# Optimization experiments

Hardware: AMD Instinct MI355X
Metric: run time of the kernel (lower is better)

Reference implementation:

```python
import jax, jax.numpy as jnp
import numpy as np

IN_FEATURES = 4096
OUT_FEATURES = 4096
NUM_GROUPS = 32
HARDTANH_MIN = -2.0
HARDTANH_MAX = 2.0
EPS = 1e-6


def setup_inputs() -> dict:
    key = jax.random.key(0)
    k1, k2 = jax.random.split(key)
    x = jax.random.normal(k1, (8192, IN_FEATURES), dtype=jnp.float32)
    W = jax.random.normal(k2, (OUT_FEATURES, IN_FEATURES), dtype=jnp.float32)
    b = jnp.zeros((OUT_FEATURES,), dtype=jnp.float32)
    return {"x": x, "W": W, "b": b}


def reference(x, W, b):
    B = x.shape[0]
    group_size = OUT_FEATURES // NUM_GROUPS
    # GEMM: y[b, n] = sum_k x[b, k] * W[n, k]
    y = jnp.einsum("bk,nk->bn", x, W)
    # GroupNorm over each group of channels per row (no affine scale)
    yg = y.reshape(B, NUM_GROUPS, group_size)
    mean = jnp.mean(yg, axis=2, keepdims=True)
    var = jnp.mean((yg - mean) ** 2, axis=2, keepdims=True)
    norm = (yg - mean) / jnp.sqrt(var + EPS)
    norm = norm.reshape(B, OUT_FEATURES) + b[None, :]
    # kernel clamps to [-2, 2], then outer clamp to [hardtanh_min, hardtanh_max]
    out = jnp.clip(norm, -2.0, 2.0)
    out = jnp.clip(out, HARDTANH_MIN, HARDTANH_MAX)
    return out
```

## Files before the change

### kernel.cpp

```cpp
#include <hip/hip_runtime.h>
#include <hip/hip_bf16.h>
#include <stdint.h>

#define M_DIM 8192
#define N_DIM 4096
#define K_DIM 4096
#define BM 128
#define BN 128
#define BK 32

typedef __attribute__((ext_vector_type(8))) short short8;
typedef __attribute__((ext_vector_type(4))) float f32x4;
typedef unsigned short ushort_t;

__device__ __forceinline__ ushort_t f2bf(float f) {
    uint32_t u = __float_as_uint(f);
    uint32_t r = (u + 0x7FFFu + ((u >> 16) & 1u)) >> 16;
    return (ushort_t)r;
}

__global__ void cvt_f32_bf16(const float4* __restrict__ in, ushort* __restrict__ out4, int n4) {
    int i = blockIdx.x * blockDim.x + threadIdx.x;
    if (i < n4) {
        float4 v = in[i];
        ushort_t a = f2bf(v.x), b = f2bf(v.y), c = f2bf(v.z), d = f2bf(v.w);
        uint32_t lo = (uint32_t)a | ((uint32_t)b << 16);
        uint32_t hi = (uint32_t)c | ((uint32_t)d << 16);
        uint2* o = reinterpret_cast<uint2*>(out4);
        o[i] = make_uint2(lo, hi);
    }
}

__device__ __forceinline__ void gload_lds16(const ushort_t* g, ushort_t* l) {
    __builtin_amdgcn_global_load_lds(
        (const __attribute__((address_space(1))) unsigned int*)g,
        (__attribute__((address_space(3))) unsigned int*)l,
        16, 0, 0);
}

__global__ __launch_bounds__(256, 2)
void gemm_gn_kernel(const ushort_t* __restrict__ xb,
                    const ushort_t* __restrict__ wb,
                    const float*   __restrict__ bias,
                    float*         __restrict__ out)
{
    __shared__ ushort_t As[BM * BK];
    __shared__ ushort_t Bs[BN * BK];
    __shared__ float redS [2][BM];
    __shared__ float redS2[2][BM];

    const int tid = threadIdx.x;
    const int w   = tid >> 6;
    const int l   = tid & 63;
    const int wr  = w >> 1;
    const int wc  = w & 1;
    const int l15 = l & 15;
    const int l4  = l >> 4;

    const int TN   = N_DIM / BN;
    const int bid  = blockIdx.x;
    const int brow = (bid / TN) * BM;
    const int bcol = (bid % TN) * BN;

    f32x4 acc[4][4];
#pragma unroll
    for (int i = 0; i < 4; ++i)
#pragma unroll
        for (int j = 0; j < 4; ++j) acc[i][j] = (f32x4){0.f, 0.f, 0.f, 0.f};

    const int srow = tid >> 2;
    const int scol = (tid & 3) * 8;
    const ushort_t* ga0 = xb + (size_t)(brow + srow)      * K_DIM + scol;
    const ushort_t* ga1 = xb + (size_t)(brow + 64 + srow) * K_DIM + scol;
    const ushort_t* gb0 = wb + (size_t)(bcol + srow)      * K_DIM + scol;
    const ushort_t* gb1 = wb + (size_t)(bcol + 64 + srow) * K_DIM + scol;
    ushort_t* lA0 = As + w * 512;
    ushort_t* lA1 = As + 2048 + w * 512;
    ushort_t* lB0 = Bs + w * 512;
    ushort_t* lB1 = Bs + 2048 + w * 512;

    const int aoff = (wr * 64 + l15) * BK + l4 * 8;
    const int boff = (wc * 64 + l15) * BK + l4 * 8;

    for (int kt = 0; kt < K_DIM / BK; ++kt) {
        const int k0 = kt * BK;
        __syncthreads();
        gload_lds16(ga0 + k0, lA0);
        gload_lds16(ga1 + k0, lA1);
        gload_lds16(gb0 + k0, lB0);
        gload_lds16(gb1 + k0, lB1);
        __syncthreads();

        short8 af[4], bf[4];
#pragma unroll
        for (int mi = 0; mi < 4; ++mi)
            af[mi] = *reinterpret_cast<const short8*>(&As[aoff + mi * 16 * BK]);
#pragma unroll
        for (int ni = 0; ni < 4; ++ni)
            bf[ni] = *reinterpret_cast<const short8*>(&Bs[boff + ni * 16 * BK]);
#pragma unroll
        for (int mi = 0; mi < 4; ++mi)
#pragma unroll
            for (int ni = 0; ni < 4; ++ni)
                acc[mi][ni] = __builtin_amdgcn_mfma_f32_16x16x32_bf16(
                    af[mi], bf[ni], acc[mi][ni], 0, 0, 0);
    }

    float s[4][4], s2[4][4];
#pragma unroll
    for (int mi = 0; mi < 4; ++mi)
#pragma unroll
        for (int r = 0; r < 4; ++r) {
            float a = 0.f, b = 0.f;
#pragma unroll
            for (int ni = 0; ni < 4; ++ni) {
                float v = acc[mi][ni][r];
                a += v;
                b += v * v;
            }
            s[mi][r] = a;
            s2[mi][r] = b;
        }
#pragma unroll
    for (int mi = 0; mi < 4; ++mi)
#pragma unroll
        for (int r = 0; r < 4; ++r) {
#pragma unroll
            for (int m = 1; m < 16; m <<= 1) {
                s[mi][r]  += __shfl_xor(s[mi][r],  m);
                s2[mi][r] += __shfl_xor(s2[mi][r], m);
            }
        }

    __syncthreads();
    if (l15 == 0) {
#pragma unroll
        for (int mi = 0; mi < 4; ++mi)
#pragma unroll
            for (int r = 0; r < 4; ++r) {
                int R = wr * 64 + mi * 16 + l4 * 4 + r;
                redS [wc][R] = s[mi][r];
                redS2[wc][R] = s2[mi][r];
            }
    }
    __syncthreads();

    float bv[4];
#pragma unroll
    for (int ni = 0; ni < 4; ++ni)
        bv[ni] = bias[bcol + wc * 64 + ni * 16 + l15];

    const float inv_gs = 1.0f / 128.0f;
#pragma unroll
    for (int mi = 0; mi < 4; ++mi)
#pragma unroll
        for (int r = 0; r < 4; ++r) {
            int R = wr * 64 + mi * 16 + l4 * 4 + r;
            float S  = redS [0][R] + redS [1][R];
            float S2 = redS2[0][R] + redS2[1][R];
            float mean = S * inv_gs;
            float var  = S2 * inv_gs - mean * mean;
            float inv  = rsqrtf(var + 1e-6f);
            size_t rowbase = (size_t)(brow + R) * N_DIM + bcol + wc * 64 + l15;
#pragma unroll
            for (int ni = 0; ni < 4; ++ni) {
                float v = (acc[mi][ni][r] - mean) * inv + bv[ni];
                v = fminf(fmaxf(v, -2.0f), 2.0f);
                out[rowbase + ni * 16] = v;
            }
        }
}

extern "C" void kernel_launch(void* const* d_in, const int* in_sizes, int n_in,
                              void* d_out, int out_size, void* d_ws, size_t ws_size,
                              hipStream_t stream) {
    const float* x = (const float*)d_in[0];
    const float* W = (const float*)d_in[1];
    const float* b = (const float*)d_in[2];
    float* out = (float*)d_out;

    ushort_t* xb = (ushort_t*)d_ws;
    ushort_t* wb = xb + (size_t)M_DIM * K_DIM;

    int n4x = M_DIM * K_DIM / 4;
    cvt_f32_bf16<<<(n4x + 255) / 256, 256, 0, stream>>>(
        (const float4*)x, xb, n4x);
    int n4w = N_DIM * K_DIM / 4;
    cvt_f32_bf16<<<(n4w + 255) / 256, 256, 0, stream>>>(
        (const float4*)W, wb, n4w);

    int grid = (M_DIM / BM) * (N_DIM / BN);
    gemm_gn_kernel<<<grid, 256, 0, stream>>>(xb, wb, b, out);
}
```

Before: 378.3 us.

## Use 256x256 tiles with triple-buffered async LDS pipeline and swizzle

Enlarges the GEMM tile to 256x256 with 512 threads (8 waves, each computing 128x64), and triple-buffers the global-to-LDS loads with explicit vmcnt waits so loads overlap MFMA work instead of sitting behind a full barrier each step. It also XOR-swizzles the LDS layout to cut bank conflicts, remaps block IDs for cache locality, and raises MFMA wave priority. In exchange it uses more registers and 96KB of LDS, which may limit occupancy, and the group-norm reduction is reorganised to combine two of four column-wave partials.

Measured after the change: 367.1 us. -3.0%, faster.

```diff
diff --git a/kernel.cpp b/kernel.cpp
--- a/kernel.cpp
+++ b/kernel.cpp
@@ -5,9 +5,10 @@
 #define M_DIM 8192
 #define N_DIM 4096
 #define K_DIM 4096
-#define BM 128
-#define BN 128
+#define BM 256
+#define BN 256
 #define BK 32
+#define NT (K_DIM / BK)
 
 typedef __attribute__((ext_vector_type(8))) short short8;
 typedef __attribute__((ext_vector_type(4))) float f32x4;
@@ -31,84 +32,107 @@
     }
 }
 
-__device__ __forceinline__ void gload_lds16(const ushort_t* g, ushort_t* l) {
+__device__ __forceinline__ void gload_lds16(const ushort_t* g, void* l) {
     __builtin_amdgcn_global_load_lds(
         (const __attribute__((address_space(1))) unsigned int*)g,
         (__attribute__((address_space(3))) unsigned int*)l,
         16, 0, 0);
 }
 
-__global__ __launch_bounds__(256, 2)
+__global__ __launch_bounds__(512, 2)
 void gemm_gn_kernel(const ushort_t* __restrict__ xb,
                     const ushort_t* __restrict__ wb,
                     const float*   __restrict__ bias,
                     float*         __restrict__ out)
 {
-    __shared__ ushort_t As[BM * BK];
-    __shared__ ushort_t Bs[BN * BK];
-    __shared__ float redS [2][BM];
-    __shared__ float redS2[2][BM];
+    __shared__ char pool[3 * 32768];
 
     const int tid = threadIdx.x;
     const int w   = tid >> 6;
     const int l   = tid & 63;
-    const int wr  = w >> 1;
-    const int wc  = w & 1;
+    const int wr  = w >> 2;
+    const int wc  = w & 3;
     const int l15 = l & 15;
     const int l4  = l >> 4;
 
-    const int TN   = N_DIM / BN;
-    const int bid  = blockIdx.x;
+    const int TN = N_DIM / BN;
+    int bid = blockIdx.x;
+    bid = (bid & 7) * ((M_DIM / BM) * TN / 8) + (bid >> 3);
     const int brow = (bid / TN) * BM;
     const int bcol = (bid % TN) * BN;
 
-    f32x4 acc[4][4];
-#pragma unroll
-    for (int i = 0; i < 4; ++i)
+    const int srow  = tid >> 2;
+    const int sslot = (tid & 3) ^ (srow & 3);
+    const ushort_t* gA0 = xb + (size_t)(brow + srow)       * K_DIM + sslot * 8;
+    const ushort_t* gA1 = xb + (size_t)(brow + 128 + srow) * K_DIM + sslot * 8;
+    const ushort_t* gB0 = wb + (size_t)(bcol + srow)       * K_DIM + sslot * 8;
+    const ushort_t* gB1 = wb + (size_t)(bcol + 128 + srow) * K_DIM + sslot * 8;
+
+    f32x4 acc[8][4];
+#pragma unroll
+    for (int i = 0; i < 8; ++i)
 #pragma unroll
         for (int j = 0; j < 4; ++j) acc[i][j] = (f32x4){0.f, 0.f, 0.f, 0.f};
 
-    const int srow = tid >> 2;
-    const int scol = (tid & 3) * 8;
-    const ushort_t* ga0 = xb + (size_t)(brow + srow)      * K_DIM + scol;
-    const ushort_t* ga1 = xb + (size_t)(brow + 64 + srow) * K_DIM + scol;
-    const ushort_t* gb0 = wb + (size_t)(bcol + srow)      * K_DIM + scol;
-    const ushort_t* gb1 = wb + (size_t)(bcol + 64 + srow) * K_DIM + scol;
-    ushort_t* lA0 = As + w * 512;
-    ushort_t* lA1 = As + 2048 + w * 512;
-    ushort_t* lB0 = Bs + w * 512;
-    ushort_t* lB1 = Bs + 2048 + w * 512;
-
-    const int aoff = (wr * 64 + l15) * BK + l4 * 8;
-    const int boff = (wc * 64 + l15) * BK + l4 * 8;
-
-    for (int kt = 0; kt < K_DIM / BK; ++kt) {
-        const int k0 = kt * BK;
-        __syncthreads();
-        gload_lds16(ga0 + k0, lA0);
-        gload_lds16(ga1 + k0, lA1);
-        gload_lds16(gb0 + k0, lB0);
-        gload_lds16(gb1 + k0, lB1);
-        __syncthreads();
-
-        short8 af[4], bf[4];
-#pragma unroll
-        for (int mi = 0; mi < 4; ++mi)
-            af[mi] = *reinterpret_cast<const short8*>(&As[aoff + mi * 16 * BK]);
+    auto STAGE = [&](char* buf, int t) {
+        const int k0 = t * BK;
+        char* ldsA = buf + w * 1024;
+        gload_lds16(gA0 + k0, ldsA);
+        gload_lds16(gA1 + k0, ldsA + 8192);
+        char* ldsB = buf + 16384 + w * 1024;
+        gload_lds16(gB0 + k0, ldsB);
+        gload_lds16(gB1 + k0, ldsB + 8192);
+    };
+
+    const int sw = ((l4 ^ (l15 & 3)) << 4);
+    const int arow0 = wr * 128 + l15;
+    const int brow0 = wc * 64 + l15;
+
+    auto COMPUTE = [&](char* buf) {
+        const char* A = buf;
+        const char* B = buf + 16384;
+        short8 af[8], bf[4];
+#pragma unroll
+        for (int mi = 0; mi < 8; ++mi)
+            af[mi] = *(const short8*)(A + (arow0 + mi * 16) * 64 + sw);
 #pragma unroll
         for (int ni = 0; ni < 4; ++ni)
-            bf[ni] = *reinterpret_cast<const short8*>(&Bs[boff + ni * 16 * BK]);
-#pragma unroll
-        for (int mi = 0; mi < 4; ++mi)
+            bf[ni] = *(const short8*)(B + (brow0 + ni * 16) * 64 + sw);
+        __builtin_amdgcn_s_setprio(1);
+#pragma unroll
+        for (int mi = 0; mi < 8; ++mi)
 #pragma unroll
             for (int ni = 0; ni < 4; ++ni)
                 acc[mi][ni] = __builtin_amdgcn_mfma_f32_16x16x32_bf16(
                     af[mi], bf[ni], acc[mi][ni], 0, 0, 0);
+        __builtin_amdgcn_s_setprio(0);
+    };
+
+    char* b0 = pool;
+    char* b1 = pool + 32768;
+    char* b2 = pool + 65536;
+    STAGE(b0, 0);
+    STAGE(b1, 1);
+    STAGE(b2, 2);
+    char* cur = b0; char* nxt = b1; char* fut = b2;
+
+    for (int t = 0; t < NT; ++t) {
+        if (t < NT - 2)       { asm volatile("s_waitcnt vmcnt(8)" ::: "memory"); }
+        else if (t == NT - 2) { asm volatile("s_waitcnt vmcnt(4)" ::: "memory"); }
+        else                  { asm volatile("s_waitcnt vmcnt(0)" ::: "memory"); }
+        asm volatile("s_barrier" ::: "memory");
+
+        COMPUTE(cur);
+
+        asm volatile("s_waitcnt lgkmcnt(0)" ::: "memory");
+        asm volatile("s_barrier" ::: "memory");
+        if (t + 3 < NT) STAGE(cur, t + 3);
+        char* tmp = cur; cur = nxt; nxt = fut; fut = tmp;
     }
 
-    float s[4][4], s2[4][4];
-#pragma unroll
-    for (int mi = 0; mi < 4; ++mi)
+    float s[8][4], s2[8][4];
+#pragma unroll
+    for (int mi = 0; mi < 8; ++mi)
 #pragma unroll
         for (int r = 0; r < 4; ++r) {
             float a = 0.f, b = 0.f;
@@ -118,29 +142,25 @@
                 a += v;
                 b += v * v;
             }
+#pragma unroll
+            for (int m = 1; m < 16; m <<= 1) {
+                a += __shfl_xor(a, m);
+                b += __shfl_xor(b, m);
+            }
             s[mi][r] = a;
             s2[mi][r] = b;
         }
-#pragma unroll
-    for (int mi = 0; mi < 4; ++mi)
-#pragma unroll
-        for (int r = 0; r < 4; ++r) {
-#pragma unroll
-            for (int m = 1; m < 16; m <<= 1) {
-                s[mi][r]  += __shfl_xor(s[mi][r],  m);
-                s2[mi][r] += __shfl_xor(s2[mi][r], m);
-            }
-        }
-
-    __syncthreads();
+
+    float* redS  = (float*)pool;
+    float* redS2 = (float*)(pool + 4096);
     if (l15 == 0) {
 #pragma unroll
-        for (int mi = 0; mi < 4; ++mi)
+        for (int mi = 0; mi < 8; ++mi)
 #pragma unroll
             for (int r = 0; r < 4; ++r) {
-                int R = wr * 64 + mi * 16 + l4 * 4 + r;
-                redS [wc][R] = s[mi][r];
-                redS2[wc][R] = s2[mi][r];
+                int R = wr * 128 + mi * 16 + l4 * 4 + r;
+                redS [R * 4 + wc] = s[mi][r];
+                redS2[R * 4 + wc] = s2[mi][r];
             }
     }
     __syncthreads();
@@ -150,14 +170,15 @@
     for (int ni = 0; ni < 4; ++ni)
         bv[ni] = bias[bcol + wc * 64 + ni * 16 + l15];
 
+    const int g2 = (wc >> 1) * 2;
     const float inv_gs = 1.0f / 128.0f;
 #pragma unroll
-    for (int mi = 0; mi < 4; ++mi)
+    for (int mi = 0; mi < 8; ++mi)
 #pragma unroll
         for (int r = 0; r < 4; ++r) {
-            int R = wr * 64 + mi * 16 + l4 * 4 + r;
-            float S  = redS [0][R] + redS [1][R];
-            float S2 = redS2[0][R] + redS2[1][R];
+            int R = wr * 128 + mi * 16 + l4 * 4 + r;
+            float S  = redS [R * 4 + g2] + redS [R * 4 + g2 + 1];
+            float S2 = redS2[R * 4 + g2] + redS2[R * 4 + g2 + 1];
             float mean = S * inv_gs;
             float var  = S2 * inv_gs - mean * mean;
             float inv  = rsqrtf(var + 1e-6f);
@@ -190,5 +211,5 @@
         (const float4*)W, wb, n4w);
 
     int grid = (M_DIM / BM) * (N_DIM / BN);
-    gemm_gn_kernel<<<grid, 256, 0, stream>>>(xb, wb, b, out);
-}
+    gemm_gn_kernel<<<grid, 512, 0, stream>>>(xb, wb, b, out);
+}
```
